# Optimization experiments

Measured on AMD Instinct MI355X. Metric: run time of the kernel, lower is better.

## Reference

```python
import jax, jax.numpy as jnp
import numpy as np

D, NH, DH, DM = 1024, 16, 64, 4096
B, S = 2, 2048
EPS = 1e-5


def _layernorm(x, w, b):
    mu = jnp.mean(x, axis=-1, keepdims=True)
    var = jnp.mean((x - mu) ** 2, axis=-1, keepdims=True)
    return (x - mu) * jax.lax.rsqrt(var + EPS) * w + b


def setup_inputs() -> dict:
    key = jax.random.key(0)
    ks = jax.random.split(key, 8)
    scale = D ** (-0.5)
    x = jax.random.normal(ks[0], (B, S, D), dtype=jnp.float32)
    WQ = jax.random.normal(ks[1], (NH, D, DH), dtype=jnp.float32) * scale
    WK = jax.random.normal(ks[2], (NH, D, DH), dtype=jnp.float32) * scale
    WV = jax.random.normal(ks[3], (NH, D, DH), dtype=jnp.float32) * scale
    WO = jax.random.normal(ks[4], (NH, DH, D), dtype=jnp.float32) * scale
    # MLP: torch Linear default init ~ U(-1/sqrt(fan_in), 1/sqrt(fan_in)); stored as [in, out]
    W1 = jax.random.uniform(ks[5], (D, DM), dtype=jnp.float32, minval=-1.0, maxval=1.0) * D ** (-0.5)
    b1 = jnp.zeros((DM,), dtype=jnp.float32)
    W2 = jax.random.uniform(ks[6], (DM, D), dtype=jnp.float32, minval=-1.0, maxval=1.0) * DM ** (-0.5)
    b2 = jnp.zeros((D,), dtype=jnp.float32)
    ln1_w = jnp.ones((D,), dtype=jnp.float32)
    ln1_b = jnp.zeros((D,), dtype=jnp.float32)
    ln2_w = jnp.ones((D,), dtype=jnp.float32)
    ln2_b = jnp.zeros((D,), dtype=jnp.float32)
    return {"x": x, "WQ": WQ, "WK": WK, "WV": WV, "WO": WO,
            "W1": W1, "b1": b1, "W2": W2, "b2": b2,
            "ln1_w": ln1_w, "ln1_b": ln1_b, "ln2_w": ln2_w, "ln2_b": ln2_b}


def reference(x, WQ, WK, WV, WO, W1, b1, W2, b2, ln1_w, ln1_b, ln2_w, ln2_b):
    s = x.shape[1]
    dh = WQ.shape[-1]
    r = x
    h = _layernorm(x, ln1_w, ln1_b)
    # batched across all heads (original loops over h; math identical)
    Q = jnp.einsum('bsd,hde->bhse', h, WQ)
    K = jnp.einsum('bsd,hde->bhse', h, WK)
    V = jnp.einsum('bsd,hde->bhse', h, WV)
    scores = jnp.einsum('bhqe,bhke->bhqk', Q, K) / jnp.sqrt(jnp.float32(dh))
    causal = jnp.tril(jnp.ones((s, s), dtype=bool))  # True = keep
    scores = jnp.where(causal, scores, -jnp.inf)
    attn = jax.nn.softmax(scores, axis=-1)
    ctx = jnp.einsum('bhqk,bhke->bhqe', attn, V)
    ao = jnp.einsum('bhqe,hed->bqd', ctx, WO)  # sum over heads
    x = r + ao
    h2 = _layernorm(x, ln2_w, ln2_b)
    mlp = jax.nn.gelu(h2 @ W1 + b1, approximate=False) @ W2 + b2
    return x + mlp
```

## Files before the change

kernel.cpp:

```cpp
#include <hip/hip_runtime.h>
#include <hip/hip_bf16.h>
#include <cstdint>

#define D_MODEL 1024
#define NHEADS 16
#define DHEAD 64
#define DMLP 4096
#define BATCH 2
#define SEQ 2048
#define ROWS (BATCH*SEQ)
#define LN_EPS 1e-5f

typedef __attribute__((ext_vector_type(8))) short short8;
typedef __attribute__((ext_vector_type(4))) float f32x4;

typedef const __attribute__((address_space(1))) uint32_t* gas_ptr;
typedef __attribute__((address_space(3))) uint32_t* las_ptr;

__device__ __forceinline__ short f2bf(float f) {
  union { float f; uint32_t u; } v; v.f = f;
  uint32_t r = v.u + 0x7FFFu + ((v.u >> 16) & 1u);
  return (short)(r >> 16);
}
__device__ __forceinline__ float bf2f(short s) {
  union { uint32_t u; float f; } v; v.u = ((uint32_t)(uint16_t)s) << 16;
  return v.f;
}

__global__ void ln_kernel(const float* __restrict__ x, const float* __restrict__ w,
                          const float* __restrict__ b, short* __restrict__ out) {
  int row = blockIdx.x;
  int t = threadIdx.x;
  const float4 v = ((const float4*)(x + (size_t)row * D_MODEL))[t];
  float s = v.x + v.y + v.z + v.w;
  float s2 = v.x*v.x + v.y*v.y + v.z*v.z + v.w*v.w;
#pragma unroll
  for (int k = 1; k < 64; k <<= 1) { s += __shfl_xor(s, k); s2 += __shfl_xor(s2, k); }
  __shared__ float red[8];
  int wv = t >> 6;
  if ((t & 63) == 0) { red[wv] = s; red[wv + 4] = s2; }
  __syncthreads();
  s = red[0] + red[1] + red[2] + red[3];
  s2 = red[4] + red[5] + red[6] + red[7];
  float mu = s * (1.0f / D_MODEL);
  float var = s2 * (1.0f / D_MODEL) - mu * mu;
  float rstd = rsqrtf(var + LN_EPS);
  const float4 wv4 = ((const float4*)w)[t];
  const float4 bv4 = ((const float4*)b)[t];
  short4 o4;
  o4.x = f2bf((v.x - mu) * rstd * wv4.x + bv4.x);
  o4.y = f2bf((v.y - mu) * rstd * wv4.y + bv4.y);
  o4.z = f2bf((v.z - mu) * rstd * wv4.z + bv4.z);
  o4.w = f2bf((v.w - mu) * rstd * wv4.w + bv4.w);
  *(short4*)(out + (size_t)row * D_MODEL + t * 4) = o4;
}

__global__ __launch_bounds__(256) void transpose_tile(const float* __restrict__ src, short* __restrict__ dst,
                                                      int R, int C, int srcMatStride) {
  __shared__ float tile[64][65];
  const int m = blockIdx.z;
  const int r0 = blockIdx.y * 64, c0 = blockIdx.x * 64;
  const int tx = threadIdx.x & 15, ty = threadIdx.x >> 4;
  const float* s = src + (size_t)m * srcMatStride + (size_t)r0 * C + c0;
#pragma unroll
  for (int i = 0; i < 4; i++) {
    float4 v = *(const float4*)(s + (size_t)(ty + i * 16) * C + tx * 4);
    tile[ty + i * 16][tx * 4 + 0] = v.x;
    tile[ty + i * 16][tx * 4 + 1] = v.y;
    tile[ty + i * 16][tx * 4 + 2] = v.z;
    tile[ty + i * 16][tx * 4 + 3] = v.w;
  }
  __syncthreads();
  short* d = dst + (size_t)m * C * R + (size_t)c0 * R + r0;
#pragma unroll
  for (int p = 0; p < 4; p++) {
    int c = ty + p * 16;
    int r4 = tx * 4;
    short4 o;
    o.x = f2bf(tile[r4 + 0][c]);
    o.y = f2bf(tile[r4 + 1][c]);
    o.z = f2bf(tile[r4 + 2][c]);
    o.w = f2bf(tile[r4 + 3][c]);
    *(short4*)(d + (size_t)c * R + r4) = o;
  }
}

template<int EPI>
__global__ __launch_bounds__(256) void gemm_bt(const short* __restrict__ A, const short* __restrict__ BT,
    const float* __restrict__ bias, const float* __restrict__ resid,
    float* __restrict__ outf, short* __restrict__ outb, float* __restrict__ part,
    int M, int N, int K, int LDA, int LDB) {
  __shared__ alignas(16) short As[3][4096];
  __shared__ alignas(16) short Bs[3][4096];
  const int t = threadIdx.x;
  const int l = t & 63, w = t >> 6;
  const int l15 = l & 15, l4 = l >> 4;
  const int row0 = blockIdx.y * 128, col0 = blockIdx.x * 128;
  if (EPI == 5) {
    A  += (size_t)blockIdx.z * K;
    BT += (size_t)blockIdx.z * K;
  }
  f32x4 acc[4][4] = {};

  const int gr = w * 16 + (l >> 2);
  const int c8 = ((l & 3) ^ ((l >> 3) & 3)) * 8;
  const short* Ab0 = A  + (size_t)(row0 + gr) * LDA + c8;
  const short* Ab1 = A  + (size_t)(row0 + 64 + gr) * LDA + c8;
  const short* Bb0 = BT + (size_t)(col0 + gr) * LDB + c8;
  const short* Bb1 = BT + (size_t)(col0 + 64 + gr) * LDB + c8;
  char* AsB = (char*)As;
  char* BsB = (char*)Bs;
  const int soff = w * 1024 + l * 16;

  auto stg = [&](int ti) {
    const int bo = (ti % 3) * 8192;
    const int k0 = ti << 5;
    __builtin_amdgcn_global_load_lds((gas_ptr)(Ab0 + k0), (las_ptr)(AsB + bo + soff),        16, 0, 0);
    __builtin_amdgcn_global_load_lds((gas_ptr)(Ab1 + k0), (las_ptr)(AsB + bo + 4096 + soff), 16, 0, 0);
    __builtin_amdgcn_global_load_lds((gas_ptr)(Bb0 + k0), (las_ptr)(BsB + bo + soff),        16, 0, 0);
    __builtin_amdgcn_global_load_lds((gas_ptr)(Bb1 + k0), (las_ptr)(BsB + bo + 4096 + soff), 16, 0, 0);
  };

  const int nk = K >> 5;
  stg(0);
  if (nk > 1) stg(1);
  asm volatile("s_waitcnt vmcnt(4)" ::: "memory");
  __builtin_amdgcn_s_barrier();

  const int wr = (w >> 1) * 64, wc = (w & 1) * 64;
  const int rch = (l4 ^ ((l15 >> 1) & 3)) * 16;
  const char* Arow = AsB + (wr >> 6) * 4096 + l15 * 64 + rch;
  const char* Brow = BsB + (wc >> 6) * 4096 + l15 * 64 + rch;

  for (int ti = 0; ti < nk; ti++) {
    const int bo = (ti % 3) * 8192;
    if (ti + 2 < nk) stg(ti + 2);
    short8 a[4], bfr[4];
#pragma unroll
    for (int m = 0; m < 4; m++) a[m]   = *(const short8*)(Arow + bo + m * 1024);
#pragma unroll
    for (int n = 0; n < 4; n++) bfr[n] = *(const short8*)(Brow + bo + n * 1024);
#pragma unroll
    for (int m = 0; m < 4; m++)
#pragma unroll
      for (int n = 0; n < 4; n++)
        acc[m][n] = __builtin_amdgcn_mfma_f32_16x16x32_bf16(a[m], bfr[n], acc[m][n], 0, 0, 0);
    if (ti + 2 < nk)      { asm volatile("s_waitcnt vmcnt(4)" ::: "memory"); }
    else if (ti + 1 < nk) { asm volatile("s_waitcnt vmcnt(0)" ::: "memory"); }
    __builtin_amdgcn_s_barrier();
  }

#pragma unroll
  for (int m = 0; m < 4; m++) {
#pragma unroll
    for (int n = 0; n < 4; n++) {
#pragma unroll
      for (int j = 0; j < 4; j++) {
        int R_ = row0 + wr + m * 16 + l4 * 4 + j;
        int C_ = col0 + wc + n * 16 + l15;
        float v = acc[m][n][j];
        size_t o = (size_t)R_ * N + C_;
        if (EPI == 0) {
          outb[o] = f2bf(v);
        } else if (EPI == 2) {
          float xx = v + bias[C_];
          outb[o] = f2bf(0.5f * xx * (1.0f + erff(xx * 0.70710678118f)));
        } else if (EPI == 5) {
          if (blockIdx.z == 0) outf[o] = v + (bias ? bias[C_] : 0.0f) + resid[o];
          else part[o] = v;
        }
      }
    }
  }
}

__global__ void reduce1(float* __restrict__ out, const float* __restrict__ p, int n4) {
  for (int i = blockIdx.x * 256 + threadIdx.x; i < n4; i += gridDim.x * 256) {
    float4 o = ((float4*)out)[i];
    float4 q = ((const float4*)p)[i];
    o.x += q.x; o.y += q.y; o.z += q.z; o.w += q.w;
    ((float4*)out)[i] = o;
  }
}

__device__ __forceinline__ void attn_step(
    int kt_, int qt, int bufP,
    const short* __restrict__ base, const short* __restrict__ vbase,
    short8& vWA, short8& vWB,
    short8& vLA, short8& vLB,
    const short8 qf[2],
    char* KsB, char* VtB, char* PlB,
    f32x4 acc[4], float mrun[4], float lrun[4],
    int w, int l, int q0, int vr, int vd0)
{
  const int l15 = l & 15, l4 = l >> 4;
  const int bufQ = bufP ^ 1;
  if (kt_ < qt) {
#pragma unroll
    for (int i = 0; i < 8; i++) {
      int d = vd0 + i;
      int cs = (vr >> 2) ^ ((d >> 3) & 7);
      uint32_t val = (uint32_t)(uint16_t)vWA[i] | ((uint32_t)(uint16_t)vWB[i] << 16);
      *(uint32_t*)(VtB + bufQ * 9216 + d * 144 + cs * 16 + (vr & 3) * 4) = val;
    }
#pragma unroll
    for (int i = 0; i < 2; i++) {
      int g = (w * 2 + i) * 64 + l;
      int key = g >> 3, ck = g & 7;
      const short* src = base + (size_t)((kt_ + 1) * 64 + key) * 3072 + 1024 + ((ck ^ (key & 7)) * 8);
      __builtin_amdgcn_global_load_lds((gas_ptr)src, (las_ptr)(KsB + bufQ * 8192 + g * 16), 16, 0, 0);
    }
  }
  if (kt_ + 2 <= qt) {
    vLA = *(const short8*)(vbase + (size_t)((kt_ + 2) * 64 + 2 * vr) * 3072);
    vLB = *(const short8*)(vbase + (size_t)((kt_ + 2) * 64 + 2 * vr + 1) * 3072);
  }

  f32x4 sc[4];
#pragma unroll
  for (int cb = 0; cb < 4; cb++) {
    f32x4 s = {};
    int key = cb * 16 + l15;
#pragma unroll
    for (int c = 0; c < 2; c++) {
      int ck = (c * 4 + l4) ^ (key & 7);
      short8 kf = *(const short8*)(KsB + bufP * 8192 + key * 128 + ck * 16);
      s = __builtin_amdgcn_mfma_f32_16x16x32_bf16(qf[c], kf, s, 0, 0, 0);
    }
    sc[cb] = s;
  }

  const bool lastt = (kt_ == qt);
  float alpha[4];
#pragma unroll
  for (int jj = 0; jj < 4; jj++) {
    int qg = q0 + l4 * 4 + jj;
    float s0 = sc[0][jj] * 0.125f;
    float s1 = sc[1][jj] * 0.125f;
    float s2 = sc[2][jj] * 0.125f;
    float s3 = sc[3][jj] * 0.125f;
    if (lastt) {
      int kg = kt_ * 64 + l15;
      if (kg      > qg) s0 = -1e30f;
      if (kg + 16 > qg) s1 = -1e30f;
      if (kg + 32 > qg) s2 = -1e30f;
      if (kg + 48 > qg) s3 = -1e30f;
    }
    float rm = fmaxf(fmaxf(s0, s1), fmaxf(s2, s3));
    rm = fmaxf(rm, __shfl_xor(rm, 1));
    rm = fmaxf(rm, __shfl_xor(rm, 2));
    rm = fmaxf(rm, __shfl_xor(rm, 4));
    rm = fmaxf(rm, __shfl_xor(rm, 8));
    float nm = fmaxf(mrun[jj], rm);
    float al = __expf(mrun[jj] - nm);
    mrun[jj] = nm;
    float p0 = __expf(s0 - nm), p1 = __expf(s1 - nm);
    float p2 = __expf(s2 - nm), p3 = __expf(s3 - nm);
    float ps = p0 + p1 + p2 + p3;
    ps += __shfl_xor(ps, 1);
    ps += __shfl_xor(ps, 2);
    ps += __shfl_xor(ps, 4);
    ps += __shfl_xor(ps, 8);
    lrun[jj] = lrun[jj] * al + ps;
    alpha[jj] = al;
    short* pr = (short*)(PlB + (l4 * 4 + jj) * 144);
    pr[l15]      = f2bf(p0);
    pr[16 + l15] = f2bf(p1);
    pr[32 + l15] = f2bf(p2);
    pr[48 + l15] = f2bf(p3);
  }
#pragma unroll
  for (int db = 0; db < 4; db++) {
    f32x4 a = acc[db];
    a[0] *= alpha[0]; a[1] *= alpha[1]; a[2] *= alpha[2]; a[3] *= alpha[3];
    acc[db] = a;
  }
#pragma unroll
  for (int kc = 0; kc < 2; kc++) {
    short8 pf = *(const short8*)(PlB + l15 * 144 + kc * 64 + l4 * 16);
#pragma unroll
    for (int db = 0; db < 4; db++) {
      int d = db * 16 + l15;
      int cs = (kc * 4 + l4) ^ ((d >> 3) & 7);
      short8 vf = *(const short8*)(VtB + bufP * 9216 + d * 144 + cs * 16);
      acc[db] = __builtin_amdgcn_mfma_f32_16x16x32_bf16(pf, vf, acc[db], 0, 0, 0);
    }
  }
}

__global__ __launch_bounds__(256) void attn_mfma(const short* __restrict__ qkv, short* __restrict__ ctx) {
  __shared__ alignas(16) short Ks[2 * 64 * 64];
  __shared__ alignas(16) short Vt[2 * 64 * 72];
  __shared__ alignas(16) short Pl[4][16 * 72];
  const int t = threadIdx.x;
  const int l = t & 63;
  const int w = t >> 6;
  const int l15 = l & 15, l4 = l >> 4;
  const int bh = blockIdx.x;
  const int b = bh >> 4, h = bh & 15;
  const int qt = (gridDim.y - 1) - blockIdx.y;
  const int q0 = qt * 64 + w * 16;

  const short* base = qkv + (size_t)b * SEQ * 3072 + h * 64;

  short8 qf[2];
#pragma unroll
  for (int c = 0; c < 2; c++)
    qf[c] = *(const short8*)(base + (size_t)(q0 + l15) * 3072 + c * 32 + l4 * 8);

  const int vr = t >> 3;
  const int vd0 = (t & 7) * 8;
  const short* vbase = base + 2048 + vd0;

  char* KsB = (char*)Ks;
  char* VtB = (char*)Vt;
  char* PlB = (char*)&Pl[w][0];

  short8 va0, vb0, va1, vb1;
  va0 = *(const short8*)(vbase + (size_t)(2 * vr) * 3072);
  vb0 = *(const short8*)(vbase + (size_t)(2 * vr + 1) * 3072);
  if (qt >= 1) {
    va1 = *(const short8*)(vbase + (size_t)(64 + 2 * vr) * 3072);
    vb1 = *(const short8*)(vbase + (size_t)(64 + 2 * vr + 1) * 3072);
  }
#pragma unroll
  for (int i = 0; i < 8; i++) {
    int d = vd0 + i;
    int cs = (vr >> 2) ^ ((d >> 3) & 7);
    uint32_t val = (uint32_t)(uint16_t)va0[i] | ((uint32_t)(uint16_t)vb0[i] << 16);
    *(uint32_t*)(VtB + d * 144 + cs * 16 + (vr & 3) * 4) = val;
  }
#pragma unroll
  for (int i = 0; i < 2; i++) {
    int g = (w * 2 + i) * 64 + l;
    int key = g >> 3, ck = g & 7;
    const short* src = base + (size_t)key * 3072 + 1024 + ((ck ^ (key & 7)) * 8);
    __builtin_amdgcn_global_load_lds((gas_ptr)src, (las_ptr)(KsB + g * 16), 16, 0, 0);
  }
  __syncthreads();

  f32x4 acc[4] = {};
  float mrun[4] = {-1e30f, -1e30f, -1e30f, -1e30f};
  float lrun[4] = {0.f, 0.f, 0.f, 0.f};

  int kt = 0;
  while (true) {
    attn_step(kt, qt, 0, base, vbase, va1, vb1, va0, vb0, qf,
              KsB, VtB, PlB, acc, mrun, lrun, w, l, q0, vr, vd0);
    __syncthreads();
    if (++kt > qt) break;
    attn_step(kt, qt, 1, base, vbase, va0, vb0, va1, vb1, qf,
              KsB, VtB, PlB, acc, mrun, lrun, w, l, q0, vr, vd0);
    __syncthreads();
    if (++kt > qt) break;
  }

  float inv[4];
#pragma unroll
  for (int jj = 0; jj < 4; jj++) inv[jj] = 1.0f / lrun[jj];
  short* obase = ctx + (size_t)(b * SEQ + q0) * D_MODEL + h * 64;
#pragma unroll
  for (int db = 0; db < 4; db++)
#pragma unroll
    for (int jj = 0; jj < 4; jj++)
      obase[(size_t)(l4 * 4 + jj) * D_MODEL + db * 16 + l15] = f2bf(acc[db][jj] * inv[jj]);
}

extern "C" void kernel_launch(void* const* d_in, const int* in_sizes, int n_in,
                              void* d_out, int out_size, void* d_ws, size_t ws_size,
                              hipStream_t stream) {
  (void)in_sizes; (void)n_in; (void)out_size; (void)ws_size;
  const float* x    = (const float*)d_in[0];
  const float* WQ   = (const float*)d_in[1];
  const float* WK   = (const float*)d_in[2];
  const float* WV   = (const float*)d_in[3];
  const float* WO   = (const float*)d_in[4];
  const float* W1   = (const float*)d_in[5];
  const float* b1   = (const float*)d_in[6];
  const float* W2   = (const float*)d_in[7];
  const float* b2   = (const float*)d_in[8];
  const float* ln1w = (const float*)d_in[9];
  const float* ln1b = (const float*)d_in[10];
  const float* ln2w = (const float*)d_in[11];
  const float* ln2b = (const float*)d_in[12];
  float* out = (float*)d_out;

  char* p = (char*)d_ws;
  short* h1    = (short*)p; p += (size_t)ROWS * D_MODEL * 2;
  short* ctx   = (short*)p; p += (size_t)ROWS * D_MODEL * 2;
  short* h2    = (short*)p; p += (size_t)ROWS * D_MODEL * 2;
  short* m1    = (short*)p; p += (size_t)ROWS * DMLP * 2;
  short* wqkvT = (short*)p; p += (size_t)3 * D_MODEL * D_MODEL * 2;
  short* woT   = (short*)p; p += (size_t)D_MODEL * D_MODEL * 2;
  short* w1T   = (short*)p; p += (size_t)D_MODEL * DMLP * 2;
  short* w2T   = (short*)p; p += (size_t)D_MODEL * DMLP * 2;
  short* qkv   = (short*)p; p += (size_t)ROWS * 3 * D_MODEL * 2;

  float* fp1 = (float*)qkv;

  transpose_tile<<<dim3(1, 16, 16), 256, 0, stream>>>(WQ, wqkvT,                   1024, 64, D_MODEL * DHEAD);
  transpose_tile<<<dim3(1, 16, 16), 256, 0, stream>>>(WK, wqkvT + 1024 * 1024,     1024, 64, D_MODEL * DHEAD);
  transpose_tile<<<dim3(1, 16, 16), 256, 0, stream>>>(WV, wqkvT + 2 * 1024 * 1024, 1024, 64, D_MODEL * DHEAD);
  transpose_tile<<<dim3(16, 16, 1), 256, 0, stream>>>(WO, woT, 1024, 1024, 0);
  transpose_tile<<<dim3(64, 16, 1), 256, 0, stream>>>(W1, w1T, 1024, 4096, 0);
  transpose_tile<<<dim3(16, 64, 1), 256, 0, stream>>>(W2, w2T, 4096, 1024, 0);

  ln_kernel<<<ROWS, 256, 0, stream>>>(x, ln1w, ln1b, h1);
  gemm_bt<0><<<dim3(3 * D_MODEL / 128, ROWS / 128), 256, 0, stream>>>(
      h1, wqkvT, nullptr, nullptr, nullptr, qkv, nullptr,
      ROWS, 3 * D_MODEL, D_MODEL, D_MODEL, D_MODEL);
  attn_mfma<<<dim3(BATCH * NHEADS, SEQ / 64), 256, 0, stream>>>(qkv, ctx);
  gemm_bt<5><<<dim3(D_MODEL / 128, ROWS / 128, 2), 256, 0, stream>>>(
      ctx, woT, nullptr, x, out, nullptr, fp1,
      ROWS, D_MODEL, D_MODEL / 2, D_MODEL, D_MODEL);
  reduce1<<<2048, 256, 0, stream>>>(out, fp1, ROWS * D_MODEL / 4);
  ln_kernel<<<ROWS, 256, 0, stream>>>(out, ln2w, ln2b, h2);
  gemm_bt<2><<<dim3(DMLP / 128, ROWS / 128), 256, 0, stream>>>(
      h2, w1T, b1, nullptr, nullptr, m1, nullptr,
      ROWS, DMLP, D_MODEL, D_MODEL, D_MODEL);
  gemm_bt<5><<<dim3(D_MODEL / 128, ROWS / 128, 2), 256, 0, stream>>>(
      m1, w2T, b2, out, out, nullptr, fp1,
      ROWS, D_MODEL, DMLP / 2, DMLP, DMLP);
  reduce1<<<2048, 256, 0, stream>>>(out, fp1, ROWS * D_MODEL / 4);
}
```

Before: 315.9 us.

## Add 256x256-tile GEMM kernel with split-K=4 for MLP down-projection

Adds a 512-thread GEMM with 256x256 output tiles, 128KB of double-buffered LDS filled by direct global-to-LDS loads, and MFMA priority hints. It replaces the QKV, MLP-up and MLP-down GEMMs. The down-projection moves from split-K 2 to split-K 4, with three partial buffers summed by a new reduce3 kernel. Larger tiles raise data reuse per block but cut occupancy and shrink the grid (e.g. 12x16 blocks for QKV), which may underfill the GPU's compute units.

```diff
diff --git a/kernel.cpp b/kernel.cpp
--- a/kernel.cpp
+++ b/kernel.cpp
@@ -86,6 +86,132 @@
 }
 
 template<int EPI>
+__global__ __launch_bounds__(512) void gemm256(const short* __restrict__ A, const short* __restrict__ BT,
+    const float* __restrict__ bias, const float* __restrict__ resid,
+    float* __restrict__ outf, short* __restrict__ outb,
+    float* __restrict__ pp1, float* __restrict__ pp2, float* __restrict__ pp3,
+    int M, int N, int K, int LDA, int LDB) {
+  extern __shared__ __align__(16) char lds[];
+  const int t = threadIdx.x;
+  const int l = t & 63, w = t >> 6;
+  const int l15 = l & 15, l4 = l >> 4;
+  const int row0 = blockIdx.y * 256, col0 = blockIdx.x * 256;
+  const int z = blockIdx.z;
+  const size_t kz = (size_t)z * K;
+  const int wrr = (w >> 2) * 128;
+  const int wc = (w & 3) * 64;
+
+  f32x4 acc[8][4] = {};
+
+  auto stage = [&](int ti, int buf) {
+    char* b0 = lds + buf * 65536;
+    const size_t ko = kz + (size_t)ti * 64;
+#pragma unroll
+    for (int i = 0; i < 4; i++) {
+      int G = (i * 8 + w) * 64 + l;
+      int gr = G >> 3, sp = G & 7;
+      const short* src = A + (size_t)(row0 + gr) * LDA + ko + ((sp ^ (gr & 7)) * 8);
+      __builtin_amdgcn_global_load_lds((gas_ptr)src, (las_ptr)(b0 + G * 16), 16, 0, 0);
+    }
+#pragma unroll
+    for (int i = 0; i < 4; i++) {
+      int G = (i * 8 + w) * 64 + l;
+      int gr = G >> 3, sp = G & 7;
+      const short* src = BT + (size_t)(col0 + gr) * LDB + ko + ((sp ^ (gr & 7)) * 8);
+      __builtin_amdgcn_global_load_lds((gas_ptr)src, (las_ptr)(b0 + 32768 + G * 16), 16, 0, 0);
+    }
+  };
+
+  stage(0, 0);
+  asm volatile("s_waitcnt vmcnt(0)" ::: "memory");
+  __builtin_amdgcn_s_barrier();
+
+  const int rs0 = ((l4) ^ (l15 & 7)) * 16;
+  const int rs1 = ((4 + l4) ^ (l15 & 7)) * 16;
+  const int nk = K >> 6;
+
+  for (int ti = 0; ti < nk; ti++) {
+    const int cur = ti & 1;
+    if (ti + 1 < nk) stage(ti + 1, cur ^ 1);
+    const char* Ab = lds + cur * 65536;
+    const char* Bb = Ab + 32768;
+    short8 af[8], bfr[4];
+#pragma unroll
+    for (int fr = 0; fr < 8; fr++) af[fr] = *(const short8*)(Ab + (wrr + fr * 16 + l15) * 128 + rs0);
+#pragma unroll
+    for (int n = 0; n < 4; n++) bfr[n] = *(const short8*)(Bb + (wc + n * 16 + l15) * 128 + rs0);
+    __builtin_amdgcn_s_setprio(1);
+#pragma unroll
+    for (int fr = 0; fr < 8; fr++)
+#pragma unroll
+      for (int n = 0; n < 4; n++)
+        acc[fr][n] = __builtin_amdgcn_mfma_f32_16x16x32_bf16(af[fr], bfr[n], acc[fr][n], 0, 0, 0);
+    __builtin_amdgcn_s_setprio(0);
+#pragma unroll
+    for (int fr = 0; fr < 8; fr++) af[fr] = *(const short8*)(Ab + (wrr + fr * 16 + l15) * 128 + rs1);
+#pragma unroll
+    for (int n = 0; n < 4; n++) bfr[n] = *(const short8*)(Bb + (wc + n * 16 + l15) * 128 + rs1);
+    __builtin_amdgcn_s_setprio(1);
+#pragma unroll
+    for (int fr = 0; fr < 8; fr++)
+#pragma unroll
+      for (int n = 0; n < 4; n++)
+        acc[fr][n] = __builtin_amdgcn_mfma_f32_16x16x32_bf16(af[fr], bfr[n], acc[fr][n], 0, 0, 0);
+    __builtin_amdgcn_s_setprio(0);
+    if (ti + 1 < nk) { asm volatile("s_waitcnt vmcnt(0)" ::: "memory"); }
+    __builtin_amdgcn_s_barrier();
+  }
+
+#pragma unroll
+  for (int fr = 0; fr < 8; fr++) {
+#pragma unroll
+    for (int fc = 0; fc < 4; fc++) {
+#pragma unroll
+      for (int j = 0; j < 4; j++) {
+        int R = row0 + wrr + fr * 16 + l4 * 4 + j;
+        int C = col0 + wc + fc * 16 + l15;
+        float v = acc[fr][fc][j];
+        size_t o = (size_t)R * N + C;
+        if (EPI == 0) {
+          outb[o] = f2bf(v);
+        } else if (EPI == 2) {
+          float xx = v + bias[C];
+          outb[o] = f2bf(0.5f * xx * (1.0f + erff(xx * 0.70710678118f)));
+        } else if (EPI == 3) {
+          if (z == 0) outf[o] = v + bias[C] + resid[o];
+          else if (z == 1) pp1[o] = v;
+          else if (z == 2) pp2[o] = v;
+          else pp3[o] = v;
+        }
+      }
+    }
+  }
+}
+
+__global__ void reduce1(float* __restrict__ out, const float* __restrict__ p, int n4) {
+  for (int i = blockIdx.x * 256 + threadIdx.x; i < n4; i += gridDim.x * 256) {
+    float4 o = ((float4*)out)[i];
+    float4 q = ((const float4*)p)[i];
+    o.x += q.x; o.y += q.y; o.z += q.z; o.w += q.w;
+    ((float4*)out)[i] = o;
+  }
+}
+__global__ void reduce3(float* __restrict__ out, const float* __restrict__ a,
+                        const float* __restrict__ b, const float* __restrict__ c, int n4) {
+  for (int i = blockIdx.x * 256 + threadIdx.x; i < n4; i += gridDim.x * 256) {
+    float4 o = ((float4*)out)[i];
+    float4 x = ((const float4*)a)[i];
+    float4 y = ((const float4*)b)[i];
+    float4 zz = ((const float4*)c)[i];
+    o.x += x.x + y.x + zz.x;
+    o.y += x.y + y.y + zz.y;
+    o.z += x.z + y.z + zz.z;
+    o.w += x.w + y.w + zz.w;
+    ((float4*)out)[i] = o;
+  }
+}
+
+template<int EPI>
 __global__ __launch_bounds__(256) void gemm_bt(const short* __restrict__ A, const short* __restrict__ BT,
     const float* __restrict__ bias, const float* __restrict__ resid,
     float* __restrict__ outf, short* __restrict__ outb, float* __restrict__ part,
@@ -171,15 +297,6 @@
         }
       }
     }
-  }
-}
-
-__global__ void reduce1(float* __restrict__ out, const float* __restrict__ p, int n4) {
-  for (int i = blockIdx.x * 256 + threadIdx.x; i < n4; i += gridDim.x * 256) {
-    float4 o = ((float4*)out)[i];
-    float4 q = ((const float4*)p)[i];
-    o.x += q.x; o.y += q.y; o.z += q.z; o.w += q.w;
-    ((float4*)out)[i] = o;
   }
 }
 
@@ -396,7 +513,13 @@
   short* w2T   = (short*)p; p += (size_t)D_MODEL * DMLP * 2;
   short* qkv   = (short*)p; p += (size_t)ROWS * 3 * D_MODEL * 2;
 
-  float* fp1 = (float*)qkv;
+  float* fp1 = (float*)h1;
+  float* fp2 = (float*)qkv;
+  float* fp3 = (float*)wqkvT;
+
+  hipFuncSetAttribute((const void*)gemm256<0>, hipFuncAttributeMaxDynamicSharedMemorySize, 131072);
+  hipFuncSetAttribute((const void*)gemm256<2>, hipFuncAttributeMaxDynamicSharedMemorySize, 131072);
+  hipFuncSetAttribute((const void*)gemm256<3>, hipFuncAttributeMaxDynamicSharedMemorySize, 131072);
 
   transpose_tile<<<dim3(1, 16, 16), 256, 0, stream>>>(WQ, wqkvT,                   1024, 64, D_MODEL * DHEAD);
   transpose_tile<<<dim3(1, 16, 16), 256, 0, stream>>>(WK, wqkvT + 1024 * 1024,     1024, 64, D_MODEL * DHEAD);
@@ -406,20 +529,20 @@
   transpose_tile<<<dim3(16, 64, 1), 256, 0, stream>>>(W2, w2T, 4096, 1024, 0);
 
   ln_kernel<<<ROWS, 256, 0, stream>>>(x, ln1w, ln1b, h1);
-  gemm_bt<0><<<dim3(3 * D_MODEL / 128, ROWS / 128), 256, 0, stream>>>(
-      h1, wqkvT, nullptr, nullptr, nullptr, qkv, nullptr,
+  gemm256<0><<<dim3(3 * D_MODEL / 256, ROWS / 256, 1), 512, 131072, stream>>>(
+      h1, wqkvT, nullptr, nullptr, nullptr, qkv, nullptr, nullptr, nullptr,
       ROWS, 3 * D_MODEL, D_MODEL, D_MODEL, D_MODEL);
   attn_mfma<<<dim3(BATCH * NHEADS, SEQ / 64), 256, 0, stream>>>(qkv, ctx);
   gemm_bt<5><<<dim3(D_MODEL / 128, ROWS / 128, 2), 256, 0, stream>>>(
-      ctx, woT, nullptr, x, out, nullptr, fp1,
+      ctx, woT, nullptr, x, out, nullptr, fp2,
       ROWS, D_MODEL, D_MODEL / 2, D_MODEL, D_MODEL);
-  reduce1<<<2048, 256, 0, stream>>>(out, fp1, ROWS * D_MODEL / 4);
+  reduce1<<<2048, 256, 0, stream>>>(out, fp2, ROWS * D_MODEL / 4);
   ln_kernel<<<ROWS, 256, 0, stream>>>(out, ln2w, ln2b, h2);
-  gemm_bt<2><<<dim3(DMLP / 128, ROWS / 128), 256, 0, stream>>>(
-      h2, w1T, b1, nullptr, nullptr, m1, nullptr,
+  gemm256<2><<<dim3(DMLP / 256, ROWS / 256, 1), 512, 131072, stream>>>(
+      h2, w1T, b1, nullptr, nullptr, m1, nullptr, nullptr, nullptr,
       ROWS, DMLP, D_MODEL, D_MODEL, D_MODEL);
-  gemm_bt<5><<<dim3(D_MODEL / 128, ROWS / 128, 2), 256, 0, stream>>>(
-      m1, w2T, b2, out, out, nullptr, fp1,
-      ROWS, D_MODEL, DMLP / 2, DMLP, DMLP);
-  reduce1<<<2048, 256, 0, stream>>>(out, fp1, ROWS * D_MODEL / 4);
-}
+  gemm256<3><<<dim3(D_MODEL / 256, ROWS / 256, 4), 512, 131072, stream>>>(
+      m1, w2T, b2, out, out, nullptr, fp1, fp2, fp3,
+      ROWS, D_MODEL, DMLP / 4, DMLP, DMLP);
+  reduce3<<<2048, 256, 0, stream>>>(out, fp1, fp2, fp3, ROWS * D_MODEL / 4);
+}
```

After: 368.4 us. +16.6%, slower.
